# Kernel optimization log

Measured on AMD Instinct MI355X. Metric: run time of the kernel, lower is better.

Reference implementation:

```python
import jax, jax.numpy as jnp
import numpy as np

N_NODES = 50000
N_EDGES = 1_600_000
D = 256
H = 8
HD = D // H
EDGE_DIM = 32


def layer_norm(x, g, b, eps=1e-5):
    mu = jnp.mean(x, axis=-1, keepdims=True)
    var = jnp.var(x, axis=-1, keepdims=True)
    return (x - mu) * jax.lax.rsqrt(var + eps) * g + b


def setup_inputs() -> dict:
    key = jax.random.key(0)
    ks = jax.random.split(key, 24)
    def lin(k, out_d, in_d):
        s = 1.0 / np.sqrt(in_d)
        kw, kb = jax.random.split(k)
        W = jax.random.uniform(kw, (out_d, in_d), jnp.float32, -s, s)
        b = jax.random.uniform(kb, (out_d,), jnp.float32, -s, s)
        return W, b
    Wq, bq = lin(ks[0], D, D)
    Wk, bk = lin(ks[1], D, D)
    Wv, bv = lin(ks[2], D, D)
    We, be = lin(ks[3], HD, EDGE_DIM)
    Wo, bo = lin(ks[4], D, D)
    W1, b1 = lin(ks[5], 4 * D, D)
    W2, b2 = lin(ks[6], D, 4 * D)
    return {
        "x": jax.random.normal(ks[7], (N_NODES, D), jnp.float32),
        "edge_index": jax.random.randint(ks[8], (2, N_EDGES), 0, N_NODES, jnp.int64 if jax.config.jax_enable_x64 else jnp.int32),
        "edge_features": jax.random.normal(ks[9], (N_EDGES, EDGE_DIM), jnp.float32),
        "edge_weights": jax.random.uniform(ks[10], (N_EDGES,), jnp.float32),
        "Wq": Wq, "bq": bq, "Wk": Wk, "bk": bk, "Wv": Wv, "bv": bv,
        "We": We, "be": be, "Wo": Wo, "bo": bo,
        "W1": W1, "b1": b1, "W2": W2, "b2": b2,
        "g1": jnp.ones((D,), jnp.float32), "be1": jnp.zeros((D,), jnp.float32),
        "g2": jnp.ones((D,), jnp.float32), "be2": jnp.zeros((D,), jnp.float32),
        "alpha": jnp.ones((1,), jnp.float32), "beta": jnp.ones((1,), jnp.float32),
    }


def reference(x, edge_index, edge_features, edge_weights,
              Wq, bq, Wk, bk, Wv, bv, We, be, Wo, bo,
              W1, b1, W2, b2, g1, be1, g2, be2, alpha, beta):
    n = x.shape[0]
    scale = HD ** (-0.5)
    src, dst = edge_index[0], edge_index[1]

    # --- pre-norm + edge-aware attention ---
    xn = layer_norm(x, g1, be1)
    q = (xn @ Wq.T + bq).reshape(n, H, HD)
    k = (xn @ Wk.T + bk).reshape(n, H, HD)
    v = (xn @ Wv.T + bv).reshape(n, H, HD)
    ep = edge_features @ We.T + be  # [E, HD], shared across heads

    # per-edge scores: sum(q[dst] * (k[src] + ep)) * scale  -> [E, H]
    scores = jnp.einsum('ehd,ehd->eh', q[dst], k[src] + ep[:, None, :]) * scale
    scores = scores * edge_weights[:, None]

    # segment softmax over incoming edges of each dst node
    smax = jax.ops.segment_max(scores, dst, num_segments=n)  # [N, H]
    e = jnp.exp(scores - smax[dst])
    ssum = jax.ops.segment_sum(e, dst, num_segments=n)
    attn_weights = e / ssum[dst]  # [E, H]

    # gather-weighted scatter aggregate: [N, H, HD]
    agg = jax.ops.segment_sum(attn_weights[:, :, None] * v[src], dst, num_segments=n)
    attn_out = agg.reshape(n, D) @ Wo.T + bo  # dropout = identity (p=0)

    x = x + alpha * attn_out

    # --- feed-forward ---
    xn2 = layer_norm(x, g2, be2)
    ff = jax.nn.gelu(xn2 @ W1.T + b1, approximate=False) @ W2.T + b2
    x = x + beta * ff
    return x, attn_weights
```

## Files before the change

kernel.cpp:

```cpp
#include <hip/hip_runtime.h>

typedef short s16x8 __attribute__((ext_vector_type(8)));
typedef float f32x4 __attribute__((ext_vector_type(4)));

static constexpr int NN = 50000;
static constexpr int NE = 1600000;

__device__ __forceinline__ unsigned short f2b(float f) {
  union { float f; unsigned u; } c; c.f = f;
  unsigned x = c.u;
  x += 0x7fffu + ((x >> 16) & 1u);
  return (unsigned short)(x >> 16);
}
__device__ __forceinline__ int clampi(int v, int lo, int hi) {
  return v < lo ? lo : (v > hi ? hi : v);
}
__device__ __forceinline__ int rdl_i(int v, int l) {
  return __builtin_amdgcn_readlane(v, l);
}
__device__ __forceinline__ float rdl_f(float v, int l) {
  union { float f; int i; } c; c.f = v;
  c.i = __builtin_amdgcn_readlane(c.i, l);
  return c.f;
}
__device__ __forceinline__ void gl_lds16(const void* g, void* l) {
  __builtin_amdgcn_global_load_lds((const __attribute__((address_space(1))) void*)g,
                                   (__attribute__((address_space(3))) void*)l, 16, 0, 0);
}

__global__ __launch_bounds__(256) void k_cvt(const float* __restrict__ s,
                                             unsigned short* __restrict__ d, int n) {
  const int i = blockIdx.x * 256 + threadIdx.x;
  if (i < n) d[i] = f2b(s[i]);
}

__global__ __launch_bounds__(256) void k_count(const int* __restrict__ dst,
                                               int* __restrict__ counts, int E) {
  const int e = blockIdx.x * 256 + threadIdx.x;
  if (e < E) atomicAdd(&counts[clampi(dst[e], 0, NN - 1)], 1);
}

__global__ __launch_bounds__(256) void k_reserve(const int* __restrict__ counts,
                                                 int* __restrict__ offs,
                                                 int* __restrict__ cursor,
                                                 int* __restrict__ counter, int n) {
  const int i = blockIdx.x * 256 + threadIdx.x;
  const int lane = threadIdx.x & 63;
  const int c = (i < n) ? counts[i] : 0;
  int pre = c;
#pragma unroll
  for (int m = 1; m < 64; m <<= 1) {
    const int t = __shfl_up(pre, m);
    if (lane >= m) pre += t;
  }
  const int wavesum = __shfl(pre, 63);
  int base = 0;
  if (lane == 0) base = atomicAdd(counter, wavesum);
  base = __shfl(base, 0);
  const int pos = base + pre - c;
  if (i < n) {
    offs[i] = pos;
    cursor[i] = pos;
  }
}

__global__ __launch_bounds__(256) void k_scatter(const int* __restrict__ dst,
                                                 int* __restrict__ cursor,
                                                 int* __restrict__ sorted, int E) {
  const int e = blockIdx.x * 256 + threadIdx.x;
  if (e < E) {
    const int p = atomicAdd(&cursor[clampi(dst[e], 0, NN - 1)], 1);
    if (p >= 0 && p < E) sorted[p] = e;
  }
}

__global__ __launch_bounds__(256) void k_ln(const float* __restrict__ x,
                                            const float* __restrict__ g,
                                            const float* __restrict__ b,
                                            unsigned short* __restrict__ out, int n) {
  const int row = blockIdx.x * 4 + (threadIdx.x >> 6);
  if (row >= n) return;
  const int lane = threadIdx.x & 63;
  float4 xv = *(const float4*)(x + (size_t)row * 256 + 4 * lane);
  float v0 = xv.x, v1 = xv.y, v2 = xv.z, v3 = xv.w;
  float s = v0 + v1 + v2 + v3;
  float ss = v0 * v0 + v1 * v1 + v2 * v2 + v3 * v3;
#pragma unroll
  for (int m = 1; m < 64; m <<= 1) {
    s += __shfl_xor(s, m);
    ss += __shfl_xor(ss, m);
  }
  const float mu = s * (1.f / 256.f);
  const float var = ss * (1.f / 256.f) - mu * mu;
  const float rs = rsqrtf(var + 1e-5f);
  float4 gv = *(const float4*)(g + 4 * lane);
  float4 bv = *(const float4*)(b + 4 * lane);
  ushort4 o;
  o.x = f2b((v0 - mu) * rs * gv.x + bv.x);
  o.y = f2b((v1 - mu) * rs * gv.y + bv.y);
  o.z = f2b((v2 - mu) * rs * gv.z + bv.z);
  o.w = f2b((v3 - mu) * rs * gv.w + bv.w);
  *(ushort4*)(out + (size_t)row * 256 + 4 * lane) = o;
}

__global__ __launch_bounds__(256) void k_attn_score(
    const float* __restrict__ q, const float* __restrict__ k,
    const float* __restrict__ We, const float* __restrict__ be,
    const int* __restrict__ src, const float* __restrict__ ew,
    const float* __restrict__ ef, const int* __restrict__ offs,
    const int* __restrict__ counts, const int* __restrict__ sorted,
    float* __restrict__ scores, float* __restrict__ mxbuf) {
  __shared__ float WeS[32][36];
  __shared__ float beS[32];
  const int t = threadIdx.x;
  for (int i = t; i < 1024; i += 256) WeS[i >> 5][i & 31] = We[i];
  if (t < 32) beS[t] = be[t];
  __syncthreads();
  const int node = blockIdx.x * 4 + (t >> 6);
  if (node >= NN) return;
  const int lane = t & 63;
  const int h = lane >> 3;
  const int s8 = lane & 7;
  const int d0 = 4 * s8;
  const float scale = 0.17677669529663689f;

  float4 qv = *(const float4*)(q + (size_t)node * 256 + 4 * lane);
  const float qarr[4] = {qv.x, qv.y, qv.z, qv.w};

  float w0 = 0.f, w1 = 0.f, w2 = 0.f, w3 = 0.f, qb = 0.f;
#pragma unroll
  for (int t8 = 0; t8 < 8; ++t8) {
#pragma unroll
    for (int u = 0; u < 4; ++u) {
      const float qj = __shfl(qarr[u], 8 * h + t8);
      const int j = 4 * t8 + u;
      w0 += qj * WeS[j][d0 + 0];
      w1 += qj * WeS[j][d0 + 1];
      w2 += qj * WeS[j][d0 + 2];
      w3 += qj * WeS[j][d0 + 3];
      qb += qj * beS[j];
    }
  }

  const int beg = clampi(offs[node], 0, NE);
  const int cnt = clampi(counts[node], 0, NE - beg);

  float mx = -3.0e38f;
  for (int c = 0; c < cnt; c += 64) {
    const int ccnt = min(64, cnt - c);
    int eid_l = 0, s_l = 0;
    float ew_l = 0.f;
    if (lane < ccnt) {
      eid_l = clampi(sorted[beg + c + lane], 0, NE - 1);
      s_l = clampi(src[eid_l], 0, NN - 1);
      ew_l = ew[eid_l];
    }
    float4 kb0 = {0, 0, 0, 0}, kb1 = {0, 0, 0, 0};
    float4 eb0 = {0, 0, 0, 0}, eb1 = {0, 0, 0, 0};
    {
      const int s0 = rdl_i(s_l, 0), e0 = rdl_i(eid_l, 0);
      kb0 = *(const float4*)(k + (size_t)s0 * 256 + 4 * lane);
      eb0 = *(const float4*)(ef + (size_t)e0 * 32 + d0);
    }
    if (ccnt > 1) {
      const int s1 = rdl_i(s_l, 1), e1 = rdl_i(eid_l, 1);
      kb1 = *(const float4*)(k + (size_t)s1 * 256 + 4 * lane);
      eb1 = *(const float4*)(ef + (size_t)e1 * 32 + d0);
    }
    for (int j = 0; j < ccnt; ++j) {
      float4 kn = kb1, en = eb1;
      if (j + 2 < ccnt) {
        const int sn = rdl_i(s_l, j + 2), enid = rdl_i(eid_l, j + 2);
        kn = *(const float4*)(k + (size_t)sn * 256 + 4 * lane);
        en = *(const float4*)(ef + (size_t)enid * 32 + d0);
      }
      const float wgt = rdl_f(ew_l, j);
      const int eid = rdl_i(eid_l, j);
      float p = qv.x * kb0.x + qv.y * kb0.y + qv.z * kb0.z + qv.w * kb0.w +
                w0 * eb0.x + w1 * eb0.y + w2 * eb0.z + w3 * eb0.w;
      p += __shfl_xor(p, 1);
      p += __shfl_xor(p, 2);
      p += __shfl_xor(p, 4);
      const float scr = (p + qb) * scale * wgt;
      mx = fmaxf(mx, scr);
      if (s8 == 0) scores[(size_t)eid * 8 + h] = scr;
      kb0 = kb1; eb0 = eb1; kb1 = kn; eb1 = en;
    }
  }
  if (s8 == 0) mxbuf[(size_t)node * 8 + h] = mx;
}

__global__ __launch_bounds__(256) void k_attn_agg(
    const unsigned short* __restrict__ v, const int* __restrict__ src,
    const int* __restrict__ offs, const int* __restrict__ counts,
    const int* __restrict__ sorted, float* __restrict__ scores,
    const float* __restrict__ mxbuf, unsigned short* __restrict__ agg) {
  const int node = blockIdx.x * 4 + (threadIdx.x >> 6);
  if (node >= NN) return;
  const int lane = threadIdx.x & 63;
  const int h = lane >> 3;

  const int beg = clampi(offs[node], 0, NE);
  const int cnt = clampi(counts[node], 0, NE - beg);
  const int end = beg + cnt;
  const float mx = mxbuf[(size_t)node * 8 + h];

  float a0 = 0.f, a1 = 0.f, a2 = 0.f, a3 = 0.f, ssum = 0.f;
  for (int c = 0; c < cnt; c += 64) {
    const int ccnt = min(64, cnt - c);
    int eid_l = 0, s_l = 0;
    if (lane < ccnt) {
      eid_l = clampi(sorted[beg + c + lane], 0, NE - 1);
      s_l = clampi(src[eid_l], 0, NN - 1);
    }
    ushort4 vb0 = {0, 0, 0, 0}, vb1 = {0, 0, 0, 0};
    float sc0 = 0.f, sc1 = 0.f;
    {
      const int s0 = rdl_i(s_l, 0), e0 = rdl_i(eid_l, 0);
      vb0 = *(const ushort4*)(v + (size_t)s0 * 256 + 4 * lane);
      sc0 = scores[(size_t)e0 * 8 + h];
    }
    if (ccnt > 1) {
      const int s1 = rdl_i(s_l, 1), e1 = rdl_i(eid_l, 1);
      vb1 = *(const ushort4*)(v + (size_t)s1 * 256 + 4 * lane);
      sc1 = scores[(size_t)e1 * 8 + h];
    }
    for (int j = 0; j < ccnt; ++j) {
      ushort4 vn = vb1;
      float scn = sc1;
      if (j + 2 < ccnt) {
        const int sn = rdl_i(s_l, j + 2), enid = rdl_i(eid_l, j + 2);
        vn = *(const ushort4*)(v + (size_t)sn * 256 + 4 * lane);
        scn = scores[(size_t)enid * 8 + h];
      }
      const float e = __expf(sc0 - mx);
      ssum += e;
      union { unsigned u; float f; } c0, c1, c2, c3;
      c0.u = ((unsigned)vb0.x) << 16; c1.u = ((unsigned)vb0.y) << 16;
      c2.u = ((unsigned)vb0.z) << 16; c3.u = ((unsigned)vb0.w) << 16;
      a0 += e * c0.f; a1 += e * c1.f; a2 += e * c2.f; a3 += e * c3.f;
      vb0 = vb1; sc0 = sc1; vb1 = vn; sc1 = scn;
    }
  }
  const float inv = (cnt > 0) ? 1.f / ssum : 0.f;
  ushort4 o;
  o.x = f2b(a0 * inv); o.y = f2b(a1 * inv); o.z = f2b(a2 * inv); o.w = f2b(a3 * inv);
  *(ushort4*)(agg + (size_t)node * 256 + 4 * lane) = o;

  const float mxh = __shfl(mx, (lane & 7) * 8);
  const float invh = __shfl(inv, (lane & 7) * 8);
  for (int i2 = beg + (lane >> 3); i2 < end; i2 += 8) {
    const int eid = clampi(sorted[i2], 0, NE - 1);
    const size_t idx = (size_t)eid * 8 + (lane & 7);
    scores[idx] = __expf(scores[idx] - mxh) * invh;
  }
}

__global__ __launch_bounds__(256) void k_gemm(
    const unsigned short* __restrict__ A, const unsigned short* __restrict__ W,
    const float* __restrict__ bias, int M, int NC, int K, int epi,
    unsigned short* __restrict__ outb, float* __restrict__ outf,
    const float* __restrict__ resf, const float* __restrict__ scal) {
  __shared__ unsigned short As[128 * 64];
  __shared__ unsigned short Bs[128 * 64];
  const int t = threadIdx.x;
  const int lane = t & 63;
  const int wv = t >> 6;
  const int wr = wv >> 1;
  const int wc = wv & 1;
  const int m0 = blockIdx.x * 128;
  const int c0 = blockIdx.y * 128;
  const int r16 = lane & 15;
  const int quad = lane >> 4;

  f32x4 acc[4][4];
#pragma unroll
  for (int i = 0; i < 4; ++i)
#pragma unroll
    for (int j = 0; j < 4; ++j) acc[i][j] = {0.f, 0.f, 0.f, 0.f};

  for (int k0 = 0; k0 < K; k0 += 64) {
#pragma unroll
    for (int i = 0; i < 4; ++i) {
      const int ob = wv * 1024 + i * 4096;
      const int o = ob + lane * 16;
      const int row = o >> 7;
      const int colb = o & 127;
      const int ra = (m0 + row < M) ? (m0 + row) : (M - 1);
      gl_lds16((const char*)A + ((size_t)ra * K + k0) * 2 + colb, (char*)As + ob);
      gl_lds16((const char*)W + ((size_t)(c0 + row) * K + k0) * 2 + colb, (char*)Bs + ob);
    }
    __syncthreads();
#pragma unroll
    for (int kk = 0; kk < 64; kk += 32) {
      s16x8 a[4], b[4];
#pragma unroll
      for (int i = 0; i < 4; ++i)
        a[i] = *(const s16x8*)(As + (wr * 64 + 16 * i + r16) * 64 + kk + quad * 8);
#pragma unroll
      for (int j = 0; j < 4; ++j)
        b[j] = *(const s16x8*)(Bs + (wc * 64 + 16 * j + r16) * 64 + kk + quad * 8);
#pragma unroll
      for (int i = 0; i < 4; ++i)
#pragma unroll
        for (int j = 0; j < 4; ++j)
          acc[i][j] = __builtin_amdgcn_mfma_f32_16x16x32_bf16(a[i], b[j], acc[i][j], 0, 0, 0);
    }
    __syncthreads();
  }

  const float sc = scal ? scal[0] : 0.f;
#pragma unroll
  for (int j = 0; j < 4; ++j) {
    const int c = c0 + wc * 64 + 16 * j + r16;
    const float bc = bias[c];
#pragma unroll
    for (int i = 0; i < 4; ++i) {
#pragma unroll
      for (int r = 0; r < 4; ++r) {
        const int m = m0 + wr * 64 + 16 * i + quad * 4 + r;
        if (m < M) {
          float f = acc[i][j][r] + bc;
          const size_t o = (size_t)m * NC + c;
          if (epi == 0) {
            outb[o] = f2b(f);
          } else if (epi == 1) {
            outf[o] = f;
          } else if (epi == 2) {
            outf[o] = resf[o] + sc * f;
          } else {
            outb[o] = f2b(0.5f * f * (1.f + erff(f * 0.70710678118654752f)));
          }
        }
      }
    }
  }
}

extern "C" void kernel_launch(void* const* d_in, const int* in_sizes, int n_in,
                              void* d_out, int out_size, void* d_ws, size_t ws_size,
                              hipStream_t stream) {
  (void)in_sizes; (void)n_in; (void)out_size; (void)ws_size;
  const float* x   = (const float*)d_in[0];
  const int* ei    = (const int*)d_in[1];
  const float* ef  = (const float*)d_in[2];
  const float* ew  = (const float*)d_in[3];
  const float* Wq  = (const float*)d_in[4];
  const float* bq  = (const float*)d_in[5];
  const float* Wk  = (const float*)d_in[6];
  const float* bk  = (const float*)d_in[7];
  const float* Wv  = (const float*)d_in[8];
  const float* bv  = (const float*)d_in[9];
  const float* We  = (const float*)d_in[10];
  const float* bel = (const float*)d_in[11];
  const float* Wo  = (const float*)d_in[12];
  const float* bo  = (const float*)d_in[13];
  const float* W1  = (const float*)d_in[14];
  const float* b1  = (const float*)d_in[15];
  const float* W2  = (const float*)d_in[16];
  const float* b2  = (const float*)d_in[17];
  const float* g1  = (const float*)d_in[18];
  const float* be1 = (const float*)d_in[19];
  const float* g2  = (const float*)d_in[20];
  const float* be2 = (const float*)d_in[21];
  const float* alpha = (const float*)d_in[22];
  const float* beta  = (const float*)d_in[23];

  char* w = (char*)d_ws;
  auto alloc = [&](size_t b) { char* p = w; w += (b + 255) & ~(size_t)255; return p; };

  int* counts          = (int*)alloc((size_t)(NN + 1) * 4);
  int* offs            = (int*)alloc((size_t)NN * 4);
  int* cursor          = (int*)alloc((size_t)NN * 4);
  int* sorted          = (int*)alloc((size_t)NE * 4);
  float* mxbuf         = (float*)alloc((size_t)NN * 8 * 4);
  unsigned short* wbf  = (unsigned short*)alloc((size_t)786432 * 2);
  unsigned short* xn   = (unsigned short*)alloc((size_t)NN * 256 * 2);
  float* qf            = (float*)alloc((size_t)NN * 256 * 4);
  float* kf            = (float*)alloc((size_t)NN * 256 * 4);
  unsigned short* vb   = (unsigned short*)alloc((size_t)NN * 256 * 2);

  unsigned short* wq_bf = wbf;
  unsigned short* wk_bf = wbf + 65536;
  unsigned short* wv_bf = wbf + 131072;
  unsigned short* wo_bf = wbf + 196608;
  unsigned short* w1_bf = wbf + 262144;
  unsigned short* w2_bf = wbf + 524288;

  unsigned short* agg = xn;
  unsigned short* xn2 = vb;
  unsigned short* h1  = (unsigned short*)qf;

  float* out_x   = (float*)d_out;
  float* scores  = (float*)d_out + (size_t)NN * 256;

  const int* src = ei;
  const int* dst = ei + NE;

  hipMemsetAsync(counts, 0, (size_t)(NN + 1) * 4, stream);
  k_count<<<dim3((NE + 255) / 256), dim3(256), 0, stream>>>(dst, counts, NE);
  k_reserve<<<dim3((NN + 255) / 256), dim3(256), 0, stream>>>(counts, offs, cursor, counts + NN, NN);
  k_scatter<<<dim3((NE + 255) / 256), dim3(256), 0, stream>>>(dst, cursor, sorted, NE);

  k_cvt<<<dim3(256), dim3(256), 0, stream>>>(Wq, wq_bf, 65536);
  k_cvt<<<dim3(256), dim3(256), 0, stream>>>(Wk, wk_bf, 65536);
  k_cvt<<<dim3(256), dim3(256), 0, stream>>>(Wv, wv_bf, 65536);
  k_cvt<<<dim3(256), dim3(256), 0, stream>>>(Wo, wo_bf, 65536);
  k_cvt<<<dim3(1024), dim3(256), 0, stream>>>(W1, w1_bf, 262144);
  k_cvt<<<dim3(1024), dim3(256), 0, stream>>>(W2, w2_bf, 262144);

  k_ln<<<dim3(NN / 4), dim3(256), 0, stream>>>(x, g1, be1, xn, NN);

  dim3 gB(256);
  dim3 gQ((NN + 127) / 128, 2);
  dim3 gF1((NN + 127) / 128, 8);
  k_gemm<<<gQ, gB, 0, stream>>>(xn, wq_bf, bq, NN, 256, 256, 1, nullptr, qf, nullptr, nullptr);
  k_gemm<<<gQ, gB, 0, stream>>>(xn, wk_bf, bk, NN, 256, 256, 1, nullptr, kf, nullptr, nullptr);
  k_gemm<<<gQ, gB, 0, stream>>>(xn, wv_bf, bv, NN, 256, 256, 0, vb, nullptr, nullptr, nullptr);

  k_attn_score<<<dim3(NN / 4), dim3(256), 0, stream>>>(qf, kf, We, bel, src, ew, ef,
                                                       offs, counts, sorted, scores, mxbuf);
  k_attn_agg<<<dim3(NN / 4), dim3(256), 0, stream>>>(vb, src, offs, counts, sorted,
                                                     scores, mxbuf, agg);

  k_gemm<<<gQ, gB, 0, stream>>>(agg, wo_bf, bo, NN, 256, 256, 2, nullptr, out_x, x, alpha);

  k_ln<<<dim3(NN / 4), dim3(256), 0, stream>>>(out_x, g2, be2, xn2, NN);

  k_gemm<<<gF1, gB, 0, stream>>>(xn2, w1_bf, b1, NN, 1024, 256, 3, h1, nullptr, nullptr, nullptr);

  k_gemm<<<gQ, gB, 0, stream>>>(h1, w2_bf, b2, NN, 256, 1024, 2, nullptr, out_x, out_x, beta);
}
```

Baseline: 1.585 ms.

## Move softmax normalization to coalesced kernel and swizzle GEMM LDS tiles

The scattered per-node rewrite of attention scores inside the aggregation kernel is replaced by a separate streaming kernel. It runs over all edges in order and reads the per-node max and inverse sum from a new invbuf, which makes the score read-modify-write coalesced at the cost of an extra launch and a gather by dst. Separately, the GEMM's LDS tiles use an XOR swizzle on the 16-byte column chunk keyed by row, to avoid bank conflicts on the MFMA operand reads.

```diff
diff --git a/kernel.cpp b/kernel.cpp
--- a/kernel.cpp
+++ b/kernel.cpp
@@ -193,16 +193,17 @@
 __global__ __launch_bounds__(256) void k_attn_agg(
     const unsigned short* __restrict__ v, const int* __restrict__ src,
     const int* __restrict__ offs, const int* __restrict__ counts,
-    const int* __restrict__ sorted, float* __restrict__ scores,
-    const float* __restrict__ mxbuf, unsigned short* __restrict__ agg) {
+    const int* __restrict__ sorted, const float* __restrict__ scores,
+    const float* __restrict__ mxbuf, float* __restrict__ invbuf,
+    unsigned short* __restrict__ agg) {
   const int node = blockIdx.x * 4 + (threadIdx.x >> 6);
   if (node >= NN) return;
   const int lane = threadIdx.x & 63;
   const int h = lane >> 3;
+  const int s8 = lane & 7;
 
   const int beg = clampi(offs[node], 0, NE);
   const int cnt = clampi(counts[node], 0, NE - beg);
-  const int end = beg + cnt;
   const float mx = mxbuf[(size_t)node * 8 + h];
 
   float a0 = 0.f, a1 = 0.f, a2 = 0.f, a3 = 0.f, ssum = 0.f;
@@ -246,14 +247,21 @@
   ushort4 o;
   o.x = f2b(a0 * inv); o.y = f2b(a1 * inv); o.z = f2b(a2 * inv); o.w = f2b(a3 * inv);
   *(ushort4*)(agg + (size_t)node * 256 + 4 * lane) = o;
-
-  const float mxh = __shfl(mx, (lane & 7) * 8);
-  const float invh = __shfl(inv, (lane & 7) * 8);
-  for (int i2 = beg + (lane >> 3); i2 < end; i2 += 8) {
-    const int eid = clampi(sorted[i2], 0, NE - 1);
-    const size_t idx = (size_t)eid * 8 + (lane & 7);
-    scores[idx] = __expf(scores[idx] - mxh) * invh;
-  }
+  if (s8 == 0) invbuf[(size_t)node * 8 + h] = inv;
+}
+
+__global__ __launch_bounds__(256) void k_norm(const int* __restrict__ dst,
+                                              const float* __restrict__ mxbuf,
+                                              const float* __restrict__ invbuf,
+                                              float* __restrict__ scores) {
+  const int idx = blockIdx.x * 256 + threadIdx.x;
+  if (idx >= NE * 8) return;
+  const int e = idx >> 3;
+  const int h = idx & 7;
+  const int node = clampi(dst[e], 0, NN - 1);
+  const float mx = mxbuf[(size_t)node * 8 + h];
+  const float inv = invbuf[(size_t)node * 8 + h];
+  scores[idx] = __expf(scores[idx] - mx) * inv;
 }
 
 __global__ __launch_bounds__(256) void k_gemm(
@@ -285,7 +293,7 @@
       const int ob = wv * 1024 + i * 4096;
       const int o = ob + lane * 16;
       const int row = o >> 7;
-      const int colb = o & 127;
+      const int colb = (o & 127) ^ ((row & 7) << 4);
       const int ra = (m0 + row < M) ? (m0 + row) : (M - 1);
       gl_lds16((const char*)A + ((size_t)ra * K + k0) * 2 + colb, (char*)As + ob);
       gl_lds16((const char*)W + ((size_t)(c0 + row) * K + k0) * 2 + colb, (char*)Bs + ob);
@@ -295,11 +303,17 @@
     for (int kk = 0; kk < 64; kk += 32) {
       s16x8 a[4], b[4];
 #pragma unroll
-      for (int i = 0; i < 4; ++i)
-        a[i] = *(const s16x8*)(As + (wr * 64 + 16 * i + r16) * 64 + kk + quad * 8);
-#pragma unroll
-      for (int j = 0; j < 4; ++j)
-        b[j] = *(const s16x8*)(Bs + (wc * 64 + 16 * j + r16) * 64 + kk + quad * 8);
+      for (int i = 0; i < 4; ++i) {
+        const int row = wr * 64 + 16 * i + r16;
+        const int cb = (kk + quad * 8) * 2;
+        a[i] = *(const s16x8*)((const char*)As + row * 128 + (cb ^ ((row & 7) << 4)));
+      }
+#pragma unroll
+      for (int j = 0; j < 4; ++j) {
+        const int row = wc * 64 + 16 * j + r16;
+        const int cb = (kk + quad * 8) * 2;
+        b[j] = *(const s16x8*)((const char*)Bs + row * 128 + (cb ^ ((row & 7) << 4)));
+      }
 #pragma unroll
       for (int i = 0; i < 4; ++i)
 #pragma unroll
@@ -374,6 +388,7 @@
   int* cursor          = (int*)alloc((size_t)NN * 4);
   int* sorted          = (int*)alloc((size_t)NE * 4);
   float* mxbuf         = (float*)alloc((size_t)NN * 8 * 4);
+  float* invbuf        = (float*)alloc((size_t)NN * 8 * 4);
   unsigned short* wbf  = (unsigned short*)alloc((size_t)786432 * 2);
   unsigned short* xn   = (unsigned short*)alloc((size_t)NN * 256 * 2);
   float* qf            = (float*)alloc((size_t)NN * 256 * 4);
@@ -421,7 +436,8 @@
   k_attn_score<<<dim3(NN / 4), dim3(256), 0, stream>>>(qf, kf, We, bel, src, ew, ef,
                                                        offs, counts, sorted, scores, mxbuf);
   k_attn_agg<<<dim3(NN / 4), dim3(256), 0, stream>>>(vb, src, offs, counts, sorted,
-                                                     scores, mxbuf, agg);
+                                                     scores, mxbuf, invbuf, agg);
+  k_norm<<<dim3((NE * 8 + 255) / 256), dim3(256), 0, stream>>>(dst, mxbuf, invbuf, scores);
 
   k_gemm<<<gQ, gB, 0, stream>>>(agg, wo_bf, bo, NN, 256, 256, 2, nullptr, out_x, x, alpha);
 
```

Result: faster. 1.546 ms (-2.5%).
